# Kernel optimization log

Measured on AMD Instinct MI355X. Metric: run time of the kernel, lower is better.

The kernel has to match this reference:

```python
import jax, jax.numpy as jnp
import numpy as np

INNER = 256   # inner_channel
NODES = 64    # nodes_num (prototypes)
EM_NUM = 3
DIAG_C = 128  # hardcoded diag_channel in FullyConnectGCLayer


def setup_inputs() -> dict:
    key = jax.random.key(0)
    ks = jax.random.split(key, 16)
    b, c, w, h = 4, 1024, 64, 64
    f32 = jnp.float32
    d = {}
    d["x"] = jax.random.normal(ks[0], (b, c, w, h), f32)
    # Conv2d weights re-initialized to N(0, 0.001) in Intra_graph.__init__
    d["W_in"] = 0.001 * jax.random.normal(ks[1], (INNER, c), f32)
    d["b_in"] = jnp.zeros((INNER,), f32)
    d["multi_proto"] = 0.001 * jax.random.normal(ks[2], (1, INNER, NODES), f32)
    d["pi0"] = jnp.ones((1, NODES), f32) / NODES
    # Conv1d layers keep default kaiming-uniform-ish init
    lim = 1.0 / np.sqrt(INNER)
    d["W_adj"] = jax.random.uniform(ks[3], (DIAG_C, INNER), f32, -lim, lim)
    d["b_adj"] = jax.random.uniform(ks[4], (DIAG_C,), f32, -lim, lim)
    d["W_diag"] = jax.random.uniform(ks[5], (DIAG_C, INNER), f32, -lim, lim)
    d["b_diag"] = jax.random.uniform(ks[6], (DIAG_C,), f32, -lim, lim)
    d["gcn_weight"] = 0.01 * jax.random.normal(ks[7], (INNER, INNER), f32)
    d["W_out"] = 0.001 * jax.random.normal(ks[8], (c, INNER), f32)
    d["b_out"] = jnp.zeros((c,), f32)
    d["gamma"] = jnp.ones((c,), f32)
    d["beta"] = jnp.zeros((c,), f32)
    d["W_out2"] = 0.001 * jax.random.normal(ks[9], (c, INNER), f32)
    d["b_out2"] = jnp.zeros((c,), f32)
    d["gamma2"] = jnp.ones((c,), f32)
    d["beta2"] = jnp.zeros((c,), f32)
    d["flag"] = 0
    return d


def _bn(y, g, bt):
    # BatchNorm2d in training mode: batch stats over (N,H,W), biased var, eps=1e-5
    m = jnp.mean(y, (0, 2, 3), keepdims=True)
    v = jnp.var(y, (0, 2, 3), keepdims=True)
    return (y - m) * jax.lax.rsqrt(v + 1e-5) * g[None, :, None, None] + bt[None, :, None, None]


def _forward(x, W_in, b_in, multi_proto, pi0, W_adj, b_adj, W_diag, b_diag,
             gcn_weight, W_out, b_out, gamma, beta, W_out2, b_out2, gamma2, beta2):
    b, c, w, h = x.shape
    wh = w * h
    x1 = (jnp.einsum('oi,bihw->bohw', W_in, x) + b_in[None, :, None, None]).reshape(b, INNER, wh)
    # ---- EM soft-clustering loop (runs under no_grad in torch) ----
    x1s = jax.lax.stop_gradient(x1)
    mu = jnp.broadcast_to(multi_proto, (b, INNER, NODES))
    pi = jnp.broadcast_to(pi0[None, :, :], (b, 1, NODES))
    for _ in range(EM_NUM):
        lik = jnp.einsum('bcm,bcn->bmn', x1s, mu)              # [b, wh, n]
        lik = jnp.exp(lik - jnp.max(lik, 2, keepdims=True))
        post = lik * pi
        post = post / (1e-18 + jnp.sum(post, 2, keepdims=True))
        prob = post / (1e-18 + jnp.sum(post, 1, keepdims=True))
        mu = jnp.einsum('bcm,bmn->bcn', x1s, prob)
        pi = jnp.sum(post, 1, keepdims=True) / wh
    post = jax.lax.stop_gradient(post)
    prob = jax.lax.stop_gradient(prob)
    # ---- aggregate to prototypes (grad flows through x1 only) ----
    x2 = jnp.einsum('bcm,bmn->bcn', x1, prob)                   # [b, inner, n]
    # ---- branch 2: scatter back, conv, bn ----
    x4 = jnp.einsum('bcn,bmn->bcm', x2, post).reshape(b, INNER, w, h)
    x4 = _bn(jnp.einsum('oi,bihw->bohw', W_out2, x4) + b_out2[None, :, None, None], gamma2, beta2)
    output2 = jax.nn.relu(jax.nn.relu(x4) + x)
    # ---- FullyConnectGCLayer on x2 ----
    xd = jnp.einsum('oi,bin->bon', W_diag, x2) + b_diag[None, :, None]
    dvec = jax.nn.sigmoid(jnp.mean(xd, 2))                      # [b, 128]
    xa = jnp.einsum('oi,bin->bon', W_adj, x2) + b_adj[None, :, None]  # [b, 128, n]
    # sigmoid(diag(d)) has 0.5 off-diagonal, sigmoid(d) on diagonal:
    # xa^T S xa = 0.5 * (1^T xa)^T (1^T xa) + xa^T diag(sig(d)-0.5) xa
    u = jnp.sum(xa, 1)                                          # [b, n]
    A = 0.5 * u[:, :, None] * u[:, None, :] + jnp.einsum('bcn,bc,bcm->bnm', xa, dvec - 0.5, xa)
    A = jax.nn.relu(A) + jnp.eye(NODES, dtype=x.dtype)[None]
    deg = jax.lax.stop_gradient(jnp.sum(A, 1) ** -0.5)          # no_grad degree, [b, n]
    A = deg[:, :, None] * A * deg[:, None, :]
    gout = jnp.einsum('oi,bin->bon', gcn_weight, jnp.einsum('bcn,bnm->bcm', x2, A))
    x2g = jax.nn.relu(gout) + x2                                # res_connect
    # ---- branch 1: scatter back, conv, bn ----
    x3 = jnp.einsum('bcn,bmn->bcm', x2g, post).reshape(b, INNER, w, h)
    x3 = _bn(jnp.einsum('oi,bihw->bohw', W_out, x3) + b_out[None, :, None, None], gamma, beta)
    output = jax.nn.relu(jax.nn.relu(x3) + x)
    return output, output2


def reference(x, W_in, b_in, multi_proto, pi0, W_adj, b_adj, W_diag, b_diag,
              gcn_weight, W_out, b_out, gamma, beta, W_out2, b_out2, gamma2, beta2, flag):
    # flag only gates a buffer EMA update (no effect on forward outputs)
    return _forward(x, W_in, b_in, multi_proto, pi0, W_adj, b_adj, W_diag, b_diag,
                    gcn_weight, W_out, b_out, gamma, beta, W_out2, b_out2, gamma2, beta2)
```

## Files before the change

### kernel.cpp

```cpp
#include <hip/hip_runtime.h>
#include <math.h>


typedef unsigned short u16;
typedef short s16x8 __attribute__((ext_vector_type(8)));
typedef float f32x4 __attribute__((ext_vector_type(4)));

constexpr int BB  = 4;
constexpr int CH  = 1024;
constexpr int IN  = 256;
constexpr int ND  = 64;
constexpr int WH  = 4096;
constexpr int DCN = 128;
constexpr size_t TOT = (size_t)BB * CH * WH;

__device__ inline u16 f2bf(float f) {
  unsigned u = __float_as_uint(f);
  return (u16)((u + 0x7fffu + ((u >> 16) & 1u)) >> 16);
}
__device__ inline float bf2f(u16 u) { return __uint_as_float((unsigned)u << 16); }
__device__ inline s16x8 ld8(const u16* p) { return *(const s16x8*)p; }
#define MFMA16(a, b, c) __builtin_amdgcn_mfma_f32_16x16x32_bf16(a, b, c, 0, 0, 0)

__global__ void k_init(const float* __restrict__ Win, const float* __restrict__ mp,
                       const float* __restrict__ pi0, u16* __restrict__ Winb,
                       u16* __restrict__ mu_t, float* __restrict__ piw,
                       float* __restrict__ sp) {
  int idx = blockIdx.x * 256 + threadIdx.x;
  if (idx < IN * CH) { Winb[idx] = f2bf(Win[idx]); return; }
  int j = idx - IN * CH;
  if (j < BB * ND * IN) {
    int bb = j >> 14, n = (j >> 8) & 63, c = j & 255;
    mu_t[((size_t)(bb * ND + n)) * IN + c] = f2bf(mp[c * ND + n]);
    return;
  }
  j -= BB * ND * IN;
  if (j < BB * ND) { piw[j] = pi0[j & 63]; return; }
  j -= BB * ND;
  if (j < 3 * BB * ND) sp[j] = 0.f;
}

__global__ __launch_bounds__(512) void k_x1(
    const float* __restrict__ x, const u16* __restrict__ Winb,
    const float* __restrict__ bin, u16* __restrict__ x1t) {
  __shared__ u16 lt[64][40];
  const int t = threadIdx.x, w = t >> 6, lr = t & 15, lg = (t >> 4) & 3;
  const int wc = w & 3, wm = w >> 2;
  const int m0 = blockIdx.x * 64, b = blockIdx.y;
  const int si = t >> 4, sm = (t & 15) * 4;
  const float* xb = x + (size_t)b * CH * WH + m0 + sm;
  f32x4 acc[4][2];
#pragma unroll
  for (int i = 0; i < 4; ++i)
#pragma unroll
    for (int j = 0; j < 2; ++j) acc[i][j] = (f32x4){0.f, 0.f, 0.f, 0.f};
  const u16* wp = Winb + (size_t)(wc * 64 + lr) * CH + lg * 8;

  float4 nxt = *(const float4*)&xb[(size_t)si * WH];
  for (int k0 = 0; k0 < CH; k0 += 32) {
    float4 cur = nxt;
    __syncthreads();
    lt[sm + 0][si] = f2bf(cur.x); lt[sm + 1][si] = f2bf(cur.y);
    lt[sm + 2][si] = f2bf(cur.z); lt[sm + 3][si] = f2bf(cur.w);
    if (k0 + 32 < CH) nxt = *(const float4*)&xb[(size_t)(k0 + 32 + si) * WH];
    __syncthreads();
    s16x8 af[4], bf[2];
#pragma unroll
    for (int i = 0; i < 4; ++i) af[i] = ld8(wp + (size_t)i * 16 * CH + k0);
#pragma unroll
    for (int j = 0; j < 2; ++j) bf[j] = *(const s16x8*)&lt[wm * 32 + j * 16 + lr][lg * 8];
#pragma unroll
    for (int i = 0; i < 4; ++i)
#pragma unroll
      for (int j = 0; j < 2; ++j) acc[i][j] = MFMA16(af[i], bf[j], acc[i][j]);
  }
#pragma unroll
  for (int i = 0; i < 4; ++i) {
    const int cb = wc * 64 + i * 16 + lg * 4;
    const float4 bi = *(const float4*)&bin[cb];
    const float bia[4] = {bi.x, bi.y, bi.z, bi.w};
#pragma unroll
    for (int j = 0; j < 2; ++j) {
      const int ml = wm * 32 + j * 16 + lr;
      float v[4];
#pragma unroll
      for (int r = 0; r < 4; ++r) v[r] = acc[i][j][r] + bia[r];
      ushort4 o;
      o.x = f2bf(v[0]); o.y = f2bf(v[1]); o.z = f2bf(v[2]); o.w = f2bf(v[3]);
      *(ushort4*)&x1t[((size_t)b * WH + m0 + ml) * IN + cb] = o;
    }
  }
}

__global__ __launch_bounds__(256) void k_em(
    const u16* __restrict__ x1t, const u16* __restrict__ mu_t,
    const float* __restrict__ piw, float* __restrict__ sp,
    u16* __restrict__ pmn, u16* __restrict__ mup16, u16* __restrict__ gp16,
    int doLast) {
  __shared__ u16 xl[256][72];
  __shared__ u16 ptl[64][72];
  const int t = threadIdx.x, w = t >> 6, lr = t & 15, lg = (t >> 4) & 3;
  const int mch = blockIdx.x, b = blockIdx.y;
  {
    f32x4 acc[4];
#pragma unroll
    for (int f = 0; f < 4; ++f) acc[f] = (f32x4){0.f, 0.f, 0.f, 0.f};
    const u16* ap = x1t + ((size_t)b * WH + mch * 64 + w * 16 + lr) * IN + lg * 8;
    const u16* bp = mu_t + ((size_t)b * ND + lr) * IN + lg * 8;
    const int ml = w * 16 + lr;
#pragma unroll
    for (int k0 = 0; k0 < IN; k0 += 32) {
      s16x8 av = ld8(ap + k0);
      const int cb = lg * 8 + k0;
#pragma unroll
      for (int e = 0; e < 8; ++e) xl[cb + e][ml] = (u16)av[e];
#pragma unroll
      for (int f = 0; f < 4; ++f)
        acc[f] = MFMA16(av, ld8(bp + f * 16 * IN + k0), acc[f]);
    }
    float pi_[4], spart[4] = {0.f, 0.f, 0.f, 0.f};
#pragma unroll
    for (int f = 0; f < 4; ++f) pi_[f] = piw[b * ND + f * 16 + lr];
#pragma unroll
    for (int r = 0; r < 4; ++r) {
      float v0 = acc[0][r], v1 = acc[1][r], v2 = acc[2][r], v3 = acc[3][r];
      float mx = fmaxf(fmaxf(v0, v1), fmaxf(v2, v3));
      mx = fmaxf(mx, __shfl_xor(mx, 1)); mx = fmaxf(mx, __shfl_xor(mx, 2));
      mx = fmaxf(mx, __shfl_xor(mx, 4)); mx = fmaxf(mx, __shfl_xor(mx, 8));
      float e0 = __expf(v0 - mx) * pi_[0], e1 = __expf(v1 - mx) * pi_[1];
      float e2 = __expf(v2 - mx) * pi_[2], e3 = __expf(v3 - mx) * pi_[3];
      float s = e0 + e1 + e2 + e3;
      s += __shfl_xor(s, 1); s += __shfl_xor(s, 2);
      s += __shfl_xor(s, 4); s += __shfl_xor(s, 8);
      const float inv = 1.f / (1e-18f + s);
      e0 *= inv; e1 *= inv; e2 *= inv; e3 *= inv;
      const int mloc = w * 16 + lg * 4 + r;
      u16 q0 = f2bf(e0), q1 = f2bf(e1), q2 = f2bf(e2), q3 = f2bf(e3);
      ptl[0 + lr][mloc]  = q0; ptl[16 + lr][mloc] = q1;
      ptl[32 + lr][mloc] = q2; ptl[48 + lr][mloc] = q3;
      if (doLast) {
        const size_t gbase = ((size_t)b * WH + mch * 64 + mloc) * ND + lr;
        pmn[gbase + 0]  = q0; pmn[gbase + 16] = q1;
        pmn[gbase + 32] = q2; pmn[gbase + 48] = q3;
      }
      spart[0] += e0; spart[1] += e1; spart[2] += e2; spart[3] += e3;
    }
#pragma unroll
    for (int f = 0; f < 4; ++f) {
      spart[f] += __shfl_xor(spart[f], 16);
      spart[f] += __shfl_xor(spart[f], 32);
    }
    if (((t >> 4) & 3) == 0) {
#pragma unroll
      for (int f = 0; f < 4; ++f)
        atomicAdd(&sp[b * ND + f * 16 + lr], spart[f]);
    }
  }
  __syncthreads();
  {
    f32x4 acc[4][4];
#pragma unroll
    for (int i = 0; i < 4; ++i)
#pragma unroll
      for (int j = 0; j < 4; ++j) acc[i][j] = (f32x4){0.f, 0.f, 0.f, 0.f};
#pragma unroll
    for (int ks = 0; ks < 2; ++ks) {
      s16x8 af[4], bf[4];
#pragma unroll
      for (int i = 0; i < 4; ++i)
        af[i] = *(const s16x8*)&xl[w * 64 + i * 16 + lr][ks * 32 + lg * 8];
#pragma unroll
      for (int j = 0; j < 4; ++j)
        bf[j] = *(const s16x8*)&ptl[j * 16 + lr][ks * 32 + lg * 8];
#pragma unroll
      for (int i = 0; i < 4; ++i)
#pragma unroll
        for (int j = 0; j < 4; ++j) acc[i][j] = MFMA16(af[i], bf[j], acc[i][j]);
    }
    u16* mo = mup16 + ((size_t)mch * BB + b) * (IN * ND);
#pragma unroll
    for (int i = 0; i < 4; ++i)
#pragma unroll
      for (int j = 0; j < 4; ++j)
#pragma unroll
        for (int r = 0; r < 4; ++r) {
          const int c = w * 64 + i * 16 + lg * 4 + r, n = j * 16 + lr;
          mo[c * ND + n] = f2bf(acc[i][j][r]);
        }
  }
  if (doLast) {
    f32x4 acc[4];
#pragma unroll
    for (int j = 0; j < 4; ++j) acc[j] = (f32x4){0.f, 0.f, 0.f, 0.f};
#pragma unroll
    for (int ks = 0; ks < 2; ++ks) {
      s16x8 av = *(const s16x8*)&ptl[w * 16 + lr][ks * 32 + lg * 8];
#pragma unroll
      for (int j = 0; j < 4; ++j) {
        s16x8 bq = *(const s16x8*)&ptl[j * 16 + lr][ks * 32 + lg * 8];
        acc[j] = MFMA16(av, bq, acc[j]);
      }
    }
    u16* go = gp16 + ((size_t)mch * BB + b) * (ND * ND);
#pragma unroll
    for (int j = 0; j < 4; ++j)
#pragma unroll
      for (int r = 0; r < 4; ++r) {
        const int n1 = w * 16 + lg * 4 + r, n2 = j * 16 + lr;
        go[n1 * ND + n2] = f2bf(acc[j][r]);
      }
  }
}

__global__ void k_mu_red(const u16* __restrict__ mup16, const float* __restrict__ spb,
                         float* __restrict__ piw, float* __restrict__ mu,
                         u16* __restrict__ mu_t, const u16* __restrict__ gp16,
                         float* __restrict__ G, int doG) {
  const int idx = blockIdx.x * 256 + threadIdx.x;
  const int bb = idx >> 14, c = (idx >> 6) & 255, n = idx & 63;
  float s = 0.f;
#pragma unroll 8
  for (int ch = 0; ch < 64; ++ch)
    s += bf2f(mup16[((size_t)ch * BB + bb) * (IN * ND) + (idx & 16383)]);
  const float v = s / (1e-18f + spb[bb * ND + n]);
  mu[idx] = v;
  mu_t[((size_t)(bb * ND + n)) * IN + c] = f2bf(v);
  if (idx < BB * ND) piw[idx] = spb[idx] * (1.f / (float)WH);
  if (doG && idx < BB * ND * ND) {
    float g = 0.f;
#pragma unroll 8
    for (int ch = 0; ch < 64; ++ch)
      g += bf2f(gp16[(size_t)ch * (BB * ND * ND) + idx]);
    G[idx] = g;
  }
}

__global__ __launch_bounds__(256) void k_gcA(
    const float* __restrict__ mu, const float* __restrict__ gw,
    const float* __restrict__ Wa, const float* __restrict__ ba,
    const float* __restrict__ Wd, const float* __restrict__ bd,
    float* __restrict__ qbuf, float* __restrict__ xabuf, float* __restrict__ dv) {
  __shared__ float sx2[IN * ND];
  __shared__ float srm[IN];
  const int t = threadIdx.x, blk = blockIdx.x, b = blockIdx.y;
  if (blk < 6) {
    const float* src = mu + (size_t)b * IN * ND;
#pragma unroll
    for (int q4 = 0; q4 < 16; ++q4)
      *(float4*)&sx2[q4 * 1024 + t * 4] = *(const float4*)&src[q4 * 1024 + t * 4];
    __syncthreads();
    const int rg = t >> 4, cg = t & 15;
    const float* W = (blk < 4) ? gw + (size_t)(blk * 64 + rg * 4) * IN
                               : Wa + (size_t)((blk - 4) * 64 + rg * 4) * IN;
    float acc[4][4] = {};
    for (int i4 = 0; i4 < 64; ++i4) {
      float4 xv[4];
#pragma unroll
      for (int e = 0; e < 4; ++e)
        xv[e] = *(const float4*)&sx2[(i4 * 4 + e) * 64 + cg * 4];
#pragma unroll
      for (int rr = 0; rr < 4; ++rr) {
        const float4 w4 = *(const float4*)&W[(size_t)rr * IN + i4 * 4];
        acc[rr][0] += w4.x * xv[0].x + w4.y * xv[1].x + w4.z * xv[2].x + w4.w * xv[3].x;
        acc[rr][1] += w4.x * xv[0].y + w4.y * xv[1].y + w4.z * xv[2].y + w4.w * xv[3].y;
        acc[rr][2] += w4.x * xv[0].z + w4.y * xv[1].z + w4.z * xv[2].z + w4.w * xv[3].z;
        acc[rr][3] += w4.x * xv[0].w + w4.y * xv[1].w + w4.z * xv[2].w + w4.w * xv[3].w;
      }
    }
    if (blk < 4) {
      float* dst = qbuf + (size_t)b * IN * ND + (size_t)(blk * 64 + rg * 4) * ND + cg * 4;
#pragma unroll
      for (int rr = 0; rr < 4; ++rr)
        *(float4*)&dst[(size_t)rr * ND] =
            make_float4(acc[rr][0], acc[rr][1], acc[rr][2], acc[rr][3]);
    } else {
      const int xr = (blk - 4) * 64 + rg * 4;
      float* dst = xabuf + (size_t)b * DCN * ND + (size_t)xr * ND + cg * 4;
#pragma unroll
      for (int rr = 0; rr < 4; ++rr) {
        const float bv = ba[xr + rr];
        *(float4*)&dst[(size_t)rr * ND] =
            make_float4(acc[rr][0] + bv, acc[rr][1] + bv, acc[rr][2] + bv, acc[rr][3] + bv);
      }
    }
  } else {
    {
      const float* row = mu + (size_t)b * IN * ND + (size_t)t * ND;
      float s = 0.f;
#pragma unroll
      for (int n4 = 0; n4 < 16; ++n4) {
        float4 v = *(const float4*)&row[n4 * 4];
        s += v.x + v.y + v.z + v.w;
      }
      srm[t] = s * (1.f / ND);
    }
    __syncthreads();
    if (t < DCN) {
      float a = 0.f;
#pragma unroll
      for (int i4 = 0; i4 < 64; ++i4) {
        float4 w4 = *(const float4*)&Wd[(size_t)t * IN + i4 * 4];
        float4 r4 = *(const float4*)&srm[i4 * 4];
        a += w4.x * r4.x + w4.y * r4.y + w4.z * r4.z + w4.w * r4.w;
      }
      a += bd[t];
      dv[b * DCN + t] = 1.f / (1.f + __expf(-a)) - 0.5f;
    }
  }
}

__global__ __launch_bounds__(256) void k_gcBC(
    const float* __restrict__ xabuf, const float* __restrict__ dv,
    const float* __restrict__ qbuf, const float* __restrict__ mu,
    float* __restrict__ x2g) {
  __shared__ float sxa[DCN * ND];
  __shared__ float sA[ND * 65];
  __shared__ float sq[64 * 68];
  __shared__ float sdv[DCN];
  __shared__ float su[ND];
  __shared__ float sdeg[ND];
  const int t = threadIdx.x, qtr = blockIdx.x, b = blockIdx.y;
  {
    const float* src = xabuf + (size_t)b * DCN * ND;
#pragma unroll
    for (int q4 = 0; q4 < 8; ++q4)
      *(float4*)&sxa[q4 * 1024 + t * 4] = *(const float4*)&src[q4 * 1024 + t * 4];
    if (t < DCN) sdv[t] = dv[b * DCN + t];
    const int r = t >> 2, seg = (t & 3) * 16;
    const float* qs = qbuf + (size_t)b * IN * ND + (size_t)(qtr * 64 + r) * ND + seg;
#pragma unroll
    for (int f = 0; f < 4; ++f) {
      float4 v = *(const float4*)&qs[f * 4];
      sq[r * 68 + seg + f * 4 + 0] = v.x; sq[r * 68 + seg + f * 4 + 1] = v.y;
      sq[r * 68 + seg + f * 4 + 2] = v.z; sq[r * 68 + seg + f * 4 + 3] = v.w;
    }
  }
  __syncthreads();
  if (t < ND) {
    float s = 0.f;
    for (int dc = 0; dc < DCN; ++dc) s += sxa[dc * ND + t];
    su[t] = s;
  }
  __syncthreads();
  {
    const int n1g = t >> 4, n2g = t & 15;
    float acc[4][4] = {};
    for (int dc = 0; dc < DCN; ++dc) {
      const float dvv = sdv[dc];
      float4 v1 = *(const float4*)&sxa[dc * ND + n1g * 4];
      const float4 v2 = *(const float4*)&sxa[dc * ND + n2g * 4];
      v1.x *= dvv; v1.y *= dvv; v1.z *= dvv; v1.w *= dvv;
      acc[0][0] += v1.x * v2.x; acc[0][1] += v1.x * v2.y;
      acc[0][2] += v1.x * v2.z; acc[0][3] += v1.x * v2.w;
      acc[1][0] += v1.y * v2.x; acc[1][1] += v1.y * v2.y;
      acc[1][2] += v1.y * v2.z; acc[1][3] += v1.y * v2.w;
      acc[2][0] += v1.z * v2.x; acc[2][1] += v1.z * v2.y;
      acc[2][2] += v1.z * v2.z; acc[2][3] += v1.z * v2.w;
      acc[3][0] += v1.w * v2.x; acc[3][1] += v1.w * v2.y;
      acc[3][2] += v1.w * v2.z; acc[3][3] += v1.w * v2.w;
    }
#pragma unroll
    for (int i = 0; i < 4; ++i) {
      const int n1 = n1g * 4 + i;
      const float u1 = su[n1];
#pragma unroll
      for (int j = 0; j < 4; ++j) {
        const int n2 = n2g * 4 + j;
        const float v = acc[i][j] + 0.5f * u1 * su[n2];
        sA[n1 * 65 + n2] = fmaxf(v, 0.f) + (n1 == n2 ? 1.f : 0.f);
      }
    }
  }
  __syncthreads();
  if (t < ND) {
    float s = 0.f;
    for (int m = 0; m < ND; ++m) s += sA[m * 65 + t];
    sdeg[t] = rsqrtf(s);
  }
  __syncthreads();
  {
    const int n1g = t >> 4, n2g = t & 15;
#pragma unroll
    for (int i = 0; i < 4; ++i) {
      const int n1 = n1g * 4 + i;
      const float dr = sdeg[n1];
#pragma unroll
      for (int e = 0; e < 4; ++e)
        sA[n1 * 65 + n2g * 4 + e] *= dr * sdeg[n2g * 4 + e];
    }
  }
  __syncthreads();
  {
    const int rg = t >> 4, cg2 = t & 15;
    float acc[4][4] = {};
    for (int k = 0; k < ND; ++k) {
      const float4 a4 = *(const float4*)&sA[k * 65 + cg2 * 4];
      float qv[4];
#pragma unroll
      for (int rr = 0; rr < 4; ++rr) qv[rr] = sq[(rg * 4 + rr) * 68 + k];
#pragma unroll
      for (int rr = 0; rr < 4; ++rr) {
        acc[rr][0] += qv[rr] * a4.x; acc[rr][1] += qv[rr] * a4.y;
        acc[rr][2] += qv[rr] * a4.z; acc[rr][3] += qv[rr] * a4.w;
      }
    }
#pragma unroll
    for (int rr = 0; rr < 4; ++rr) {
      const size_t off = (size_t)b * IN * ND + (size_t)(qtr * 64 + rg * 4 + rr) * ND + cg2 * 4;
      const float4 xv = *(const float4*)&mu[off];
      float4 o;
      o.x = fmaxf(acc[rr][0], 0.f) + xv.x; o.y = fmaxf(acc[rr][1], 0.f) + xv.y;
      o.z = fmaxf(acc[rr][2], 0.f) + xv.z; o.w = fmaxf(acc[rr][3], 0.f) + xv.w;
      *(float4*)&x2g[off] = o;
    }
  }
}

__global__ __launch_bounds__(256) void k_zdual(
    const float* __restrict__ Wo, const float* __restrict__ v1,
    float* __restrict__ z1o, u16* __restrict__ zb1o,
    const float* __restrict__ Wo2, const float* __restrict__ v2,
    float* __restrict__ z2o, u16* __restrict__ zb2o) {
  const float* W = blockIdx.z ? Wo2 : Wo;
  const float* v = blockIdx.z ? v2 : v1;
  float* z  = blockIdx.z ? z2o : z1o;
  u16* zb   = blockIdx.z ? zb2o : zb1o;
  __shared__ float As[16][68];
  __shared__ float Bs[16][64];
  const int t = threadIdx.x, tx = t & 15, ty = t >> 4;
  const int o0 = blockIdx.x * 64, bb = blockIdx.y;
  const int aoo = t >> 2, akq = (t & 3) * 4;
  const int bkk = t >> 4, bnq = (t & 15) * 4;
  float acc[4][4] = {};
  for (int k0 = 0; k0 < IN; k0 += 16) {
    {
      float4 w4 = *(const float4*)&W[(size_t)(o0 + aoo) * IN + k0 + akq];
      As[akq + 0][aoo] = w4.x; As[akq + 1][aoo] = w4.y;
      As[akq + 2][aoo] = w4.z; As[akq + 3][aoo] = w4.w;
    }
    *(float4*)&Bs[bkk][bnq] = *(const float4*)&v[((size_t)bb * IN + k0 + bkk) * ND + bnq];
    __syncthreads();
#pragma unroll
    for (int kk = 0; kk < 16; ++kk) {
      float4 a4 = *(const float4*)&As[kk][ty * 4];
      float4 b4 = *(const float4*)&Bs[kk][tx * 4];
      float ar[4] = {a4.x, a4.y, a4.z, a4.w}, br[4] = {b4.x, b4.y, b4.z, b4.w};
#pragma unroll
      for (int i = 0; i < 4; ++i)
#pragma unroll
        for (int j = 0; j < 4; ++j) acc[i][j] += ar[i] * br[j];
    }
    __syncthreads();
  }
#pragma unroll
  for (int i = 0; i < 4; ++i) {
    float4 r = make_float4(acc[i][0], acc[i][1], acc[i][2], acc[i][3]);
    const size_t off = ((size_t)bb * CH + o0 + ty * 4 + i) * ND + tx * 4;
    *(float4*)&z[off] = r;
    ushort4 h;
    h.x = f2bf(r.x); h.y = f2bf(r.y); h.z = f2bf(r.z); h.w = f2bf(r.w);
    *(ushort4*)&zb[off] = h;
  }
}

__global__ __launch_bounds__(256) void k_stats(
    const float* __restrict__ z1, const float* __restrict__ z2,
    const float* __restrict__ sp, const float* __restrict__ G,
    const float* __restrict__ gam, const float* __restrict__ bet,
    const float* __restrict__ gam2, const float* __restrict__ bet2,
    float* __restrict__ abc) {
  const int t = threadIdx.x;
  const int o = blockIdx.x * 4 + (t >> 6), lane = t & 63;
#pragma unroll
  for (int br = 0; br < 2; ++br) {
    const float* z = br ? z2 : z1;
    float macc = 0.f, eacc = 0.f;
    for (int bb = 0; bb < BB; ++bb) {
      const float zv = z[((size_t)bb * CH + o) * ND + lane];
      float s1 = zv * sp[bb * ND + lane];
      const float* Gb = G + (size_t)bb * ND * ND;
      float gz = 0.f;
      for (int k = 0; k < ND; ++k) {
        const float zk = __shfl(zv, k);
        gz += Gb[k * ND + lane] * zk;
      }
      float q = zv * gz;
#pragma unroll
      for (int off = 32; off; off >>= 1) {
        s1 += __shfl_xor(s1, off);
        q  += __shfl_xor(q, off);
      }
      macc += s1; eacc += q;
    }
    const float inv = 1.f / (float)((size_t)BB * WH);
    const float mean = macc * inv;
    const float var  = eacc * inv - mean * mean;
    const float a = (br ? gam2[o] : gam[o]) * rsqrtf(var + 1e-5f);
    const float c = (br ? bet2[o] : bet[o]) - mean * a;
    if (lane == 0) { abc[br * 2 * CH + o] = a; abc[br * 2 * CH + CH + o] = c; }
  }
}

__global__ __launch_bounds__(256) void k_epi(
    const u16* __restrict__ zb1, const u16* __restrict__ zb2,
    const u16* __restrict__ post, const float* __restrict__ abc,
    const float* __restrict__ x, float* __restrict__ out1, float* __restrict__ out2) {
  const int t = threadIdx.x, w = t >> 6, lr = t & 15, lg = (t >> 4) & 3;
  const int m0 = blockIdx.x * 256 + w * 64, o0 = blockIdx.y * 64, bb = blockIdx.z;
  f32x4 acc1[4][4], acc2[4][4];
#pragma unroll
  for (int i = 0; i < 4; ++i)
#pragma unroll
    for (int j = 0; j < 4; ++j) {
      acc1[i][j] = (f32x4){0.f, 0.f, 0.f, 0.f};
      acc2[i][j] = (f32x4){0.f, 0.f, 0.f, 0.f};
    }
  const u16* z1p = zb1 + ((size_t)bb * CH + o0 + lr) * ND + lg * 8;
  const u16* z2p = zb2 + ((size_t)bb * CH + o0 + lr) * ND + lg * 8;
  const u16* pp  = post + ((size_t)bb * WH + m0 + lr) * ND + lg * 8;
#pragma unroll
  for (int ks = 0; ks < 2; ++ks) {
    s16x8 a1[4], a2[4], bq[4];
#pragma unroll
    for (int i = 0; i < 4; ++i) {
      a1[i] = ld8(z1p + i * 16 * ND + ks * 32);
      a2[i] = ld8(z2p + i * 16 * ND + ks * 32);
    }
#pragma unroll
    for (int j = 0; j < 4; ++j) bq[j] = ld8(pp + j * 16 * ND + ks * 32);
#pragma unroll
    for (int i = 0; i < 4; ++i)
#pragma unroll
      for (int j = 0; j < 4; ++j) {
        acc1[i][j] = MFMA16(a1[i], bq[j], acc1[i][j]);
        acc2[i][j] = MFMA16(a2[i], bq[j], acc2[i][j]);
      }
  }
#pragma unroll
  for (int i = 0; i < 4; ++i)
#pragma unroll
    for (int r = 0; r < 4; ++r) {
      const int o = o0 + i * 16 + lg * 4 + r;
      const float a1v = abc[o], c1v = abc[CH + o];
      const float a2v = abc[2 * CH + o], c2v = abc[3 * CH + o];
      const size_t base = ((size_t)bb * CH + o) * WH + m0 + lr;
#pragma unroll
      for (int j = 0; j < 4; ++j) {
        const size_t off = base + j * 16;
        const float xv = x[off];
        out1[off] = fmaxf(fmaxf(a1v * acc1[i][j][r] + c1v, 0.f) + xv, 0.f);
        out2[off] = fmaxf(fmaxf(a2v * acc2[i][j][r] + c2v, 0.f) + xv, 0.f);
      }
    }
}

extern "C" void kernel_launch(void* const* d_in, const int* in_sizes, int n_in,
                              void* d_out, int out_size, void* d_ws, size_t ws_size,
                              hipStream_t stream) {
  (void)in_sizes; (void)n_in; (void)out_size; (void)ws_size;
  const float* x    = (const float*)d_in[0];
  const float* Win  = (const float*)d_in[1];
  const float* bin  = (const float*)d_in[2];
  const float* mp   = (const float*)d_in[3];
  const float* pi0  = (const float*)d_in[4];
  const float* Wa   = (const float*)d_in[5];
  const float* ba   = (const float*)d_in[6];
  const float* Wd   = (const float*)d_in[7];
  const float* bd   = (const float*)d_in[8];
  const float* gw   = (const float*)d_in[9];
  const float* Wo   = (const float*)d_in[10];
  const float* gam  = (const float*)d_in[12];
  const float* bet  = (const float*)d_in[13];
  const float* Wo2  = (const float*)d_in[14];
  const float* gam2 = (const float*)d_in[16];
  const float* bet2 = (const float*)d_in[17];

  char* ob = (char*)d_out;
  char* wp = (char*)d_ws;
  u16*   mup16 = (u16*)(ob + 0);
  u16*   gp16  = (u16*)(ob + 8388608);
  float* z1    = (float*)(ob + 10485760);
  float* z2    = (float*)(ob + 11534336);
  u16*   x1t   = (u16*)(wp + 8388608);
  u16*   Winb  = (u16*)(wp + 16777216);
  u16*   mu_t  = (u16*)(wp + 17301504);
  u16*   pmn   = (u16*)(wp + 17432576);
  float* mu    = (float*)(wp + 19529728);
  float* x2g   = (float*)(wp + 19791872);
  u16*   zb1   = (u16*)(wp + 20054016);
  u16*   zb2   = (u16*)(wp + 20578304);
  float* sp3   = (float*)(wp + 21102592);
  float* piw   = (float*)(wp + 21105664);
  float* abc   = (float*)(wp + 21106688);
  float* G     = (float*)(wp + 21123072);
  float* qbuf  = (float*)(wp + 21188608);
  float* xabuf = (float*)(wp + 21450752);
  float* dvb   = (float*)(wp + 21581824);
  float* out1  = (float*)d_out;
  float* out2  = out1 + TOT;

  k_init<<<dim3(1284), 256, 0, stream>>>(Win, mp, pi0, Winb, mu_t, piw, sp3);
  k_x1<<<dim3(64, BB), 512, 0, stream>>>(x, Winb, bin, x1t);
  for (int it = 0; it < 3; ++it) {
    float* spb = sp3 + it * 256;
    const int doLast = (it == 2);
    k_em<<<dim3(64, BB), 256, 0, stream>>>(x1t, mu_t, piw, spb, pmn,
                                           mup16, gp16, doLast);
    k_mu_red<<<dim3(256), 256, 0, stream>>>(mup16, spb, piw, mu, mu_t,
                                            gp16, G, doLast);
  }
  k_gcA<<<dim3(7, BB), 256, 0, stream>>>(mu, gw, Wa, ba, Wd, bd, qbuf, xabuf, dvb);
  k_gcBC<<<dim3(4, BB), 256, 0, stream>>>(xabuf, dvb, qbuf, mu, x2g);
  k_zdual<<<dim3(16, BB, 2), 256, 0, stream>>>(Wo, x2g, z1, zb1, Wo2, mu, z2, zb2);
  k_stats<<<dim3(256), 256, 0, stream>>>(z1, z2, sp3 + 512, G, gam, bet, gam2, bet2, abc);
  k_epi<<<dim3(16, 16, BB), 256, 0, stream>>>(zb1, zb2, pmn, abc, x, out1, out2);
}
```

Measured before the change: 224.0 us.

## Overlap branch-2 output GEMM with graph-conv prep kernel

The branch-2 output projection (Wo2 applied to mu) depends only on mu, so it is moved out of the dual z kernel and run by extra blocks of the gcA kernel. The branch-1 projection stays in a separate smaller kernel after gcBC. This shortens the serial chain by running independent work alongside the small gcA stage. In exchange, every block of the merged kernel reserves 65KB of shared memory, which limits how many z blocks can share a CU.

```diff
diff --git a/kernel.cpp b/kernel.cpp
--- a/kernel.cpp
+++ b/kernel.cpp
@@ -235,77 +235,125 @@
   }
 }
 
-__global__ __launch_bounds__(256) void k_gcA(
+__device__ void zg_body(const float* __restrict__ W, const float* __restrict__ v,
+                        float* __restrict__ z, u16* __restrict__ zb,
+                        int o0, int bb, int t, char* smem) {
+  float (*As)[68] = (float(*)[68])smem;
+  float (*Bs)[64] = (float(*)[64])(smem + 4352);
+  const int tx = t & 15, ty = t >> 4;
+  const int aoo = t >> 2, akq = (t & 3) * 4;
+  const int bkk = t >> 4, bnq = (t & 15) * 4;
+  float acc[4][4] = {};
+  for (int k0 = 0; k0 < IN; k0 += 16) {
+    {
+      float4 w4 = *(const float4*)&W[(size_t)(o0 + aoo) * IN + k0 + akq];
+      As[akq + 0][aoo] = w4.x; As[akq + 1][aoo] = w4.y;
+      As[akq + 2][aoo] = w4.z; As[akq + 3][aoo] = w4.w;
+    }
+    *(float4*)&Bs[bkk][bnq] = *(const float4*)&v[((size_t)bb * IN + k0 + bkk) * ND + bnq];
+    __syncthreads();
+#pragma unroll
+    for (int kk = 0; kk < 16; ++kk) {
+      float4 a4 = *(const float4*)&As[kk][ty * 4];
+      float4 b4 = *(const float4*)&Bs[kk][tx * 4];
+      float ar[4] = {a4.x, a4.y, a4.z, a4.w}, br[4] = {b4.x, b4.y, b4.z, b4.w};
+#pragma unroll
+      for (int i = 0; i < 4; ++i)
+#pragma unroll
+        for (int j = 0; j < 4; ++j) acc[i][j] += ar[i] * br[j];
+    }
+    __syncthreads();
+  }
+#pragma unroll
+  for (int i = 0; i < 4; ++i) {
+    float4 r = make_float4(acc[i][0], acc[i][1], acc[i][2], acc[i][3]);
+    const size_t off = ((size_t)bb * CH + o0 + ty * 4 + i) * ND + tx * 4;
+    *(float4*)&z[off] = r;
+    ushort4 h;
+    h.x = f2bf(r.x); h.y = f2bf(r.y); h.z = f2bf(r.z); h.w = f2bf(r.w);
+    *(ushort4*)&zb[off] = h;
+  }
+}
+
+__global__ __launch_bounds__(256) void k_gcAz2(
     const float* __restrict__ mu, const float* __restrict__ gw,
     const float* __restrict__ Wa, const float* __restrict__ ba,
     const float* __restrict__ Wd, const float* __restrict__ bd,
-    float* __restrict__ qbuf, float* __restrict__ xabuf, float* __restrict__ dv) {
-  __shared__ float sx2[IN * ND];
-  __shared__ float srm[IN];
-  const int t = threadIdx.x, blk = blockIdx.x, b = blockIdx.y;
-  if (blk < 6) {
-    const float* src = mu + (size_t)b * IN * ND;
-#pragma unroll
-    for (int q4 = 0; q4 < 16; ++q4)
-      *(float4*)&sx2[q4 * 1024 + t * 4] = *(const float4*)&src[q4 * 1024 + t * 4];
-    __syncthreads();
-    const int rg = t >> 4, cg = t & 15;
-    const float* W = (blk < 4) ? gw + (size_t)(blk * 64 + rg * 4) * IN
-                               : Wa + (size_t)((blk - 4) * 64 + rg * 4) * IN;
-    float acc[4][4] = {};
-    for (int i4 = 0; i4 < 64; ++i4) {
-      float4 xv[4];
-#pragma unroll
-      for (int e = 0; e < 4; ++e)
-        xv[e] = *(const float4*)&sx2[(i4 * 4 + e) * 64 + cg * 4];
-#pragma unroll
-      for (int rr = 0; rr < 4; ++rr) {
-        const float4 w4 = *(const float4*)&W[(size_t)rr * IN + i4 * 4];
-        acc[rr][0] += w4.x * xv[0].x + w4.y * xv[1].x + w4.z * xv[2].x + w4.w * xv[3].x;
-        acc[rr][1] += w4.x * xv[0].y + w4.y * xv[1].y + w4.z * xv[2].y + w4.w * xv[3].y;
-        acc[rr][2] += w4.x * xv[0].z + w4.y * xv[1].z + w4.z * xv[2].z + w4.w * xv[3].z;
-        acc[rr][3] += w4.x * xv[0].w + w4.y * xv[1].w + w4.z * xv[2].w + w4.w * xv[3].w;
-      }
-    }
-    if (blk < 4) {
-      float* dst = qbuf + (size_t)b * IN * ND + (size_t)(blk * 64 + rg * 4) * ND + cg * 4;
-#pragma unroll
-      for (int rr = 0; rr < 4; ++rr)
-        *(float4*)&dst[(size_t)rr * ND] =
-            make_float4(acc[rr][0], acc[rr][1], acc[rr][2], acc[rr][3]);
+    float* __restrict__ qbuf, float* __restrict__ xabuf, float* __restrict__ dv,
+    const float* __restrict__ Wo2, float* __restrict__ z2, u16* __restrict__ zb2) {
+  __shared__ __align__(16) char smem[66560];
+  const int t = threadIdx.x, bid = blockIdx.x;
+  if (bid < 28) {
+    const int blk = bid % 7, b = bid / 7;
+    float* sx2 = (float*)smem;
+    float* srm = (float*)(smem + 65536);
+    if (blk < 6) {
+      const float* src = mu + (size_t)b * IN * ND;
+#pragma unroll
+      for (int q4 = 0; q4 < 16; ++q4)
+        *(float4*)&sx2[q4 * 1024 + t * 4] = *(const float4*)&src[q4 * 1024 + t * 4];
+      __syncthreads();
+      const int rg = t >> 4, cg = t & 15;
+      const float* W = (blk < 4) ? gw + (size_t)(blk * 64 + rg * 4) * IN
+                                 : Wa + (size_t)((blk - 4) * 64 + rg * 4) * IN;
+      float acc[4][4] = {};
+      for (int i4 = 0; i4 < 64; ++i4) {
+        float4 xv[4];
+#pragma unroll
+        for (int e = 0; e < 4; ++e)
+          xv[e] = *(const float4*)&sx2[(i4 * 4 + e) * 64 + cg * 4];
+#pragma unroll
+        for (int rr = 0; rr < 4; ++rr) {
+          const float4 w4 = *(const float4*)&W[(size_t)rr * IN + i4 * 4];
+          acc[rr][0] += w4.x * xv[0].x + w4.y * xv[1].x + w4.z * xv[2].x + w4.w * xv[3].x;
+          acc[rr][1] += w4.x * xv[0].y + w4.y * xv[1].y + w4.z * xv[2].y + w4.w * xv[3].y;
+          acc[rr][2] += w4.x * xv[0].z + w4.y * xv[1].z + w4.z * xv[2].z + w4.w * xv[3].z;
+          acc[rr][3] += w4.x * xv[0].w + w4.y * xv[1].w + w4.z * xv[2].w + w4.w * xv[3].w;
+        }
+      }
+      if (blk < 4) {
+        float* dst = qbuf + (size_t)b * IN * ND + (size_t)(blk * 64 + rg * 4) * ND + cg * 4;
+#pragma unroll
+        for (int rr = 0; rr < 4; ++rr)
+          *(float4*)&dst[(size_t)rr * ND] =
+              make_float4(acc[rr][0], acc[rr][1], acc[rr][2], acc[rr][3]);
+      } else {
+        const int xr = (blk - 4) * 64 + rg * 4;
+        float* dst = xabuf + (size_t)b * DCN * ND + (size_t)xr * ND + cg * 4;
+#pragma unroll
+        for (int rr = 0; rr < 4; ++rr) {
+          const float bv = ba[xr + rr];
+          *(float4*)&dst[(size_t)rr * ND] =
+              make_float4(acc[rr][0] + bv, acc[rr][1] + bv, acc[rr][2] + bv, acc[rr][3] + bv);
+        }
+      }
     } else {
-      const int xr = (blk - 4) * 64 + rg * 4;
-      float* dst = xabuf + (size_t)b * DCN * ND + (size_t)xr * ND + cg * 4;
-#pragma unroll
-      for (int rr = 0; rr < 4; ++rr) {
-        const float bv = ba[xr + rr];
-        *(float4*)&dst[(size_t)rr * ND] =
-            make_float4(acc[rr][0] + bv, acc[rr][1] + bv, acc[rr][2] + bv, acc[rr][3] + bv);
-      }
-    }
-  } else {
-    {
-      const float* row = mu + (size_t)b * IN * ND + (size_t)t * ND;
-      float s = 0.f;
-#pragma unroll
-      for (int n4 = 0; n4 < 16; ++n4) {
-        float4 v = *(const float4*)&row[n4 * 4];
-        s += v.x + v.y + v.z + v.w;
-      }
-      srm[t] = s * (1.f / ND);
-    }
-    __syncthreads();
-    if (t < DCN) {
-      float a = 0.f;
-#pragma unroll
-      for (int i4 = 0; i4 < 64; ++i4) {
-        float4 w4 = *(const float4*)&Wd[(size_t)t * IN + i4 * 4];
-        float4 r4 = *(const float4*)&srm[i4 * 4];
-        a += w4.x * r4.x + w4.y * r4.y + w4.z * r4.z + w4.w * r4.w;
-      }
-      a += bd[t];
-      dv[b * DCN + t] = 1.f / (1.f + __expf(-a)) - 0.5f;
-    }
+      {
+        const float* row = mu + (size_t)b * IN * ND + (size_t)t * ND;
+        float s = 0.f;
+#pragma unroll
+        for (int n4 = 0; n4 < 16; ++n4) {
+          float4 v = *(const float4*)&row[n4 * 4];
+          s += v.x + v.y + v.z + v.w;
+        }
+        srm[t] = s * (1.f / ND);
+      }
+      __syncthreads();
+      if (t < DCN) {
+        float a = 0.f;
+#pragma unroll
+        for (int i4 = 0; i4 < 64; ++i4) {
+          float4 w4 = *(const float4*)&Wd[(size_t)t * IN + i4 * 4];
+          float4 r4 = *(const float4*)&srm[i4 * 4];
+          a += w4.x * r4.x + w4.y * r4.y + w4.z * r4.z + w4.w * r4.w;
+        }
+        a += bd[t];
+        dv[b * DCN + t] = 1.f / (1.f + __expf(-a)) - 0.5f;
+      }
+    }
+  } else if (bid >= 32 && bid < 96) {
+    const int zid = bid - 32;
+    zg_body(Wo2, mu, z2, zb2, (zid & 15) * 64, zid >> 4, t, smem);
   }
 }
 
@@ -416,51 +464,11 @@
   }
 }
 
-__global__ __launch_bounds__(256) void k_zdual(
-    const float* __restrict__ Wo, const float* __restrict__ v1,
-    float* __restrict__ z1o, u16* __restrict__ zb1o,
-    const float* __restrict__ Wo2, const float* __restrict__ v2,
-    float* __restrict__ z2o, u16* __restrict__ zb2o) {
-  const float* W = blockIdx.z ? Wo2 : Wo;
-  const float* v = blockIdx.z ? v2 : v1;
-  float* z  = blockIdx.z ? z2o : z1o;
-  u16* zb   = blockIdx.z ? zb2o : zb1o;
-  __shared__ float As[16][68];
-  __shared__ float Bs[16][64];
-  const int t = threadIdx.x, tx = t & 15, ty = t >> 4;
-  const int o0 = blockIdx.x * 64, bb = blockIdx.y;
-  const int aoo = t >> 2, akq = (t & 3) * 4;
-  const int bkk = t >> 4, bnq = (t & 15) * 4;
-  float acc[4][4] = {};
-  for (int k0 = 0; k0 < IN; k0 += 16) {
-    {
-      float4 w4 = *(const float4*)&W[(size_t)(o0 + aoo) * IN + k0 + akq];
-      As[akq + 0][aoo] = w4.x; As[akq + 1][aoo] = w4.y;
-      As[akq + 2][aoo] = w4.z; As[akq + 3][aoo] = w4.w;
-    }
-    *(float4*)&Bs[bkk][bnq] = *(const float4*)&v[((size_t)bb * IN + k0 + bkk) * ND + bnq];
-    __syncthreads();
-#pragma unroll
-    for (int kk = 0; kk < 16; ++kk) {
-      float4 a4 = *(const float4*)&As[kk][ty * 4];
-      float4 b4 = *(const float4*)&Bs[kk][tx * 4];
-      float ar[4] = {a4.x, a4.y, a4.z, a4.w}, br[4] = {b4.x, b4.y, b4.z, b4.w};
-#pragma unroll
-      for (int i = 0; i < 4; ++i)
-#pragma unroll
-        for (int j = 0; j < 4; ++j) acc[i][j] += ar[i] * br[j];
-    }
-    __syncthreads();
-  }
-#pragma unroll
-  for (int i = 0; i < 4; ++i) {
-    float4 r = make_float4(acc[i][0], acc[i][1], acc[i][2], acc[i][3]);
-    const size_t off = ((size_t)bb * CH + o0 + ty * 4 + i) * ND + tx * 4;
-    *(float4*)&z[off] = r;
-    ushort4 h;
-    h.x = f2bf(r.x); h.y = f2bf(r.y); h.z = f2bf(r.z); h.w = f2bf(r.w);
-    *(ushort4*)&zb[off] = h;
-  }
+__global__ __launch_bounds__(256) void k_zg(
+    const float* __restrict__ W, const float* __restrict__ v,
+    float* __restrict__ z, u16* __restrict__ zb) {
+  __shared__ __align__(16) char smem[8448];
+  zg_body(W, v, z, zb, blockIdx.x * 64, blockIdx.y, threadIdx.x, smem);
 }
 
 __global__ __launch_bounds__(256) void k_stats(
@@ -609,9 +617,10 @@
     k_mu_red<<<dim3(256), 256, 0, stream>>>(mup16, spb, piw, mu, mu_t,
                                             gp16, G, doLast);
   }
-  k_gcA<<<dim3(7, BB), 256, 0, stream>>>(mu, gw, Wa, ba, Wd, bd, qbuf, xabuf, dvb);
+  k_gcAz2<<<dim3(96), 256, 0, stream>>>(mu, gw, Wa, ba, Wd, bd, qbuf, xabuf, dvb,
+                                        Wo2, z2, zb2);
   k_gcBC<<<dim3(4, BB), 256, 0, stream>>>(xabuf, dvb, qbuf, mu, x2g);
-  k_zdual<<<dim3(16, BB, 2), 256, 0, stream>>>(Wo, x2g, z1, zb1, Wo2, mu, z2, zb2);
+  k_zg<<<dim3(16, BB), 256, 0, stream>>>(Wo, x2g, z1, zb1);
   k_stats<<<dim3(256), 256, 0, stream>>>(z1, z2, sp3 + 512, G, gam, bet, gam2, bet2, abc);
   k_epi<<<dim3(16, 16, BB), 256, 0, stream>>>(zb1, zb2, pmn, abc, x, out1, out2);
 }
```

After: 240.2 us. +7.2%, slower.
